# Performance work log

Hardware: AMD Instinct MI355X
Metric: run time of the kernel (lower is better)

## Reference

```python
import jax, jax.numpy as jnp
import numpy as np

N = 100000
R = 32
E = 3200000
EMB = 128
H = 32
B = 16
C = 16

def setup_inputs() -> dict:
    key = jax.random.key(0)
    ks = jax.random.split(key, 10)
    def xavier(k, shape):
        fan_in, fan_out = shape[-2], shape[-1]
        gain = jnp.sqrt(2.0)  # relu gain
        std = gain * jnp.sqrt(2.0 / (fan_in + fan_out))
        return jax.random.normal(k, shape, jnp.float32) * std
    return {
        'embeddings': xavier(ks[0], (N, EMB)),
        'comps1': xavier(ks[1], (R, B)),
        'bases1': xavier(ks[2], (B, EMB, H)),
        'comps2': xavier(ks[3], (R, B)),
        'bases2': xavier(ks[4], (B, H, C)),
        'bias1': jnp.zeros((H,), jnp.float32),
        'bias2': jnp.zeros((C,), jnp.float32),
        'rel': jax.random.randint(ks[5], (E,), 0, R, jnp.int32),
        'fr': jax.random.randint(ks[6], (E,), 0, N, jnp.int32),
        'to': jax.random.randint(ks[7], (E,), 0, N, jnp.int32),
    }

def reference(embeddings, comps1, bases1, comps2, bases2, bias1, bias2, rel, fr, to):
    n, emb = embeddings.shape
    r = comps1.shape[0]
    h = bases1.shape[2]
    # edge normalization: vals = 1 / rowsum of vertical adjacency, row = rel*n + fr
    seg = rel * n + fr  # [E]
    deg = jax.ops.segment_sum(jnp.ones_like(fr, jnp.float32), seg, num_segments=r * n)
    vals = 1.0 / deg[seg]  # [E]
    # layer 1: basis-composed weights, per-relation transform, hor-graph spmm
    w1 = jnp.einsum('rb,beh->reh', comps1, bases1)          # [r,emb,h]
    xw = jnp.einsum('ne,reh->rnh', embeddings, w1)           # [r,n,h]
    # hor_graph @ xw.view(r*n,h): hidden1[fr] += vals * xw[rel, to]
    hidden1 = jax.ops.segment_sum(vals[:, None] * xw[rel, to], fr, num_segments=n)  # [n,h]
    hidden1 = jax.nn.relu(hidden1 + bias1)
    # layer 2: ver-graph spmm then relation-combining einsum
    w2 = jnp.einsum('rb,bhc->rhc', comps2, bases2)           # [r,h,c]
    hidden2 = jax.ops.segment_sum(vals[:, None] * hidden1[to], seg, num_segments=r * n)
    hidden2 = hidden2.reshape(r, n, h)
    out = jnp.einsum('rhc,rnh->nc', w2, hidden2)             # [n,c]
    return out + bias2
```

## Files before the change

### kernel.cpp

```cpp
#include <hip/hip_runtime.h>

#define N_NODES 100000
#define N_PAD   100096
#define E_EDGES 3200000
#define NB      392
#define BCAP    12288
#define EPB     2048

typedef float f32x4 __attribute__((ext_vector_type(4)));
typedef __bf16 bf16x8 __attribute__((ext_vector_type(8)));

__device__ __forceinline__ float b2f(unsigned int u) {
    union { unsigned int i; float f; } x; x.i = u << 16; return x.f;
}
__device__ __forceinline__ unsigned short f2b(float f) {
    union { float f; unsigned int i; } x; x.f = f;
    unsigned int u = x.i + 0x7FFFu + ((x.i >> 16) & 1u);
    return (unsigned short)(u >> 16);
}

__global__ __launch_bounds__(256) void kcur(int* __restrict__ gCursor) {
    int id = blockIdx.x * 256 + threadIdx.x;
    if (id < NB) gCursor[id] = id * BCAP;
}

__global__ __launch_bounds__(256) void kemb(const float* __restrict__ emb,
                                            unsigned short* __restrict__ embb) {
    int id = blockIdx.x * 256 + threadIdx.x;
    if (id >= N_PAD * 128 / 8) return;
    size_t base = (size_t)id * 8;
    ushort4 o0 = {0, 0, 0, 0}, o1 = {0, 0, 0, 0};
    if (base < (size_t)N_NODES * 128) {
        float4 v0 = *(const float4*)(emb + base);
        float4 v1 = *(const float4*)(emb + base + 4);
        o0.x = f2b(v0.x); o0.y = f2b(v0.y); o0.z = f2b(v0.z); o0.w = f2b(v0.w);
        o1.x = f2b(v1.x); o1.y = f2b(v1.y); o1.z = f2b(v1.z); o1.w = f2b(v1.w);
    }
    *(ushort4*)(embb + base) = o0;
    *(ushort4*)(embb + base + 4) = o1;
}

__global__ __launch_bounds__(256) void kw1(const float* __restrict__ comps1,
                                           const float* __restrict__ bases1,
                                           unsigned short* __restrict__ w1T) {
    int id = blockIdx.x * 256 + threadIdx.x;
    if (id >= 1024 * 128) return;
    int k = id & 127, j = id >> 7;
    int r = j >> 5, h = j & 31;
    float s = 0.f;
#pragma unroll
    for (int b = 0; b < 16; b++)
        s += comps1[r * 16 + b] * bases1[b * 4096 + k * 32 + h];
    w1T[(size_t)j * 128 + k] = f2b(s);
}

__global__ __launch_bounds__(256) void kw2(const float* __restrict__ comps2,
                                           const float* __restrict__ bases2,
                                           unsigned short* __restrict__ w2T) {
    int id = blockIdx.x * 256 + threadIdx.x;
    if (id >= 512 * 32) return;
    int h = id & 31, j = id >> 5;
    int r = j >> 4, c = j & 15;
    float s = 0.f;
#pragma unroll
    for (int b = 0; b < 16; b++)
        s += comps2[r * 16 + b] * bases2[b * 512 + h * 16 + c];
    w2T[(size_t)j * 32 + h] = f2b(s);
}

__global__ __launch_bounds__(256) void kbinA(const int* __restrict__ rel,
                                             const int* __restrict__ fr,
                                             const int* __restrict__ to,
                                             int* __restrict__ gCursor,
                                             unsigned int* __restrict__ stage) {
    __shared__ int cnt[NB];
    __shared__ int base[NB];
    int tid = threadIdx.x;
    int g0 = blockIdx.x * (EPB / 4);
    for (int i = tid; i < NB; i += 256) cnt[i] = 0;
    __syncthreads();
#pragma unroll
    for (int i = 0; i < EPB / 1024; i++) {
        int g = g0 + i * 256 + tid;
        if (g < E_EDGES / 4) {
            int4 f4 = ((const int4*)fr)[g];
            atomicAdd(&cnt[f4.x >> 8], 1);
            atomicAdd(&cnt[f4.y >> 8], 1);
            atomicAdd(&cnt[f4.z >> 8], 1);
            atomicAdd(&cnt[f4.w >> 8], 1);
        }
    }
    __syncthreads();
    for (int i = tid; i < NB; i += 256) {
        base[i] = atomicAdd(&gCursor[i], cnt[i]);
        cnt[i] = 0;
    }
    __syncthreads();
#pragma unroll
    for (int i = 0; i < EPB / 1024; i++) {
        int g = g0 + i * 256 + tid;
        if (g < E_EDGES / 4) {
            int4 f4 = ((const int4*)fr)[g];
            int4 r4 = ((const int4*)rel)[g];
            int4 t4 = ((const int4*)to)[g];
            int fa[4] = {f4.x, f4.y, f4.z, f4.w};
            int ra[4] = {r4.x, r4.y, r4.z, r4.w};
            int ta[4] = {t4.x, t4.y, t4.z, t4.w};
#pragma unroll
            for (int u = 0; u < 4; u++) {
                int b = fa[u] >> 8;
                int rank = atomicAdd(&cnt[b], 1);
                stage[base[b] + rank] =
                    ((unsigned int)(fa[u] & 255) << 22) | ((unsigned int)ra[u] << 17) | (unsigned int)ta[u];
            }
        }
    }
}

__global__ __launch_bounds__(512) void kscan(const int* __restrict__ gCursor,
                                             int* __restrict__ bucketBase) {
    __shared__ int a[512], b[512];
    int t = threadIdx.x;
    int v = (t < NB) ? (gCursor[t] - t * BCAP) : 0;
    a[t] = v;
    __syncthreads();
    int* src = a; int* dst = b;
    for (int ofs = 1; ofs < 512; ofs <<= 1) {
        int x = src[t];
        if (t >= ofs) x += src[t - ofs];
        __syncthreads();
        dst[t] = x;
        __syncthreads();
        int* tmp = src; src = dst; dst = tmp;
    }
    if (t < NB) bucketBase[t] = src[t] - v;
}

__global__ __launch_bounds__(256) void kscatter2(const unsigned int* __restrict__ stage,
                                                 const int* __restrict__ gCursor,
                                                 const int* __restrict__ bucketBase,
                                                 int* __restrict__ rowptr,
                                                 unsigned int* __restrict__ packed) {
    __shared__ int hist[256], hexcl[256], rk[256], sa[256], sb[256];
    __shared__ int hist2[256 * 32];
    int b = blockIdx.x, t = threadIdx.x;
    int nb = gCursor[b] - b * BCAP;
    int sbase = b * BCAP;
    int gbase = bucketBase[b];
    int nb4 = nb >> 2;
    hist[t] = 0; rk[t] = 0;
    for (int i = t; i < 256 * 32; i += 256) hist2[i] = 0;
    __syncthreads();
    for (int i4 = t; i4 < nb4; i4 += 256) {
        uint4 p4 = ((const uint4*)(stage + sbase))[i4];
        unsigned int pa[4] = {p4.x, p4.y, p4.z, p4.w};
#pragma unroll
        for (int u = 0; u < 4; u++) {
            atomicAdd(&hist[pa[u] >> 22], 1);
            atomicAdd(&hist2[((pa[u] >> 22) << 5) | ((pa[u] >> 17) & 31)], 1);
        }
    }
    for (int i = (nb4 << 2) + t; i < nb; i += 256) {
        unsigned int pk = stage[sbase + i];
        atomicAdd(&hist[pk >> 22], 1);
        atomicAdd(&hist2[((pk >> 22) << 5) | ((pk >> 17) & 31)], 1);
    }
    __syncthreads();
    int v = hist[t];
    sa[t] = v;
    __syncthreads();
    int* src = sa; int* dst = sb;
    for (int ofs = 1; ofs < 256; ofs <<= 1) {
        int x = src[t];
        if (t >= ofs) x += src[t - ofs];
        __syncthreads();
        dst[t] = x;
        __syncthreads();
        int* tmp = src; src = dst; dst = tmp;
    }
    int excl = src[t] - v;
    hexcl[t] = excl;
    rowptr[b * 256 + t] = gbase + excl;
    __syncthreads();
    for (int i4 = t; i4 < nb4; i4 += 256) {
        uint4 p4 = ((const uint4*)(stage + sbase))[i4];
        unsigned int pa[4] = {p4.x, p4.y, p4.z, p4.w};
#pragma unroll
        for (int u = 0; u < 4; u++) {
            int frlo = pa[u] >> 22;
            int rank = atomicAdd(&rk[frlo], 1);
            int dg = min(hist2[(frlo << 5) | ((pa[u] >> 17) & 31)], 1023);
            packed[gbase + hexcl[frlo] + rank] = ((unsigned int)dg << 22) | (pa[u] & 0x3FFFFFu);
        }
    }
    for (int i = (nb4 << 2) + t; i < nb; i += 256) {
        unsigned int pk = stage[sbase + i];
        int frlo = pk >> 22;
        int rank = atomicAdd(&rk[frlo], 1);
        int dg = min(hist2[(frlo << 5) | ((pk >> 17) & 31)], 1023);
        packed[gbase + hexcl[frlo] + rank] = ((unsigned int)dg << 22) | (pk & 0x3FFFFFu);
    }
}

__global__ __launch_bounds__(256) void gemm1(const unsigned short* __restrict__ embb,
                                             const unsigned short* __restrict__ w1T,
                                             unsigned short* __restrict__ xw) {
    __shared__ unsigned short ldsT[4 * 16 * 136];
    int id = blockIdx.x;
    int xcd = id & 7, w = id >> 3;
    int bn = w & 15, mgl = w >> 4;
    int mg = mgl * 8 + xcd;
    if (mg >= 98) return;
    int lane = threadIdx.x & 63, wave = threadIdx.x >> 6;
    int m_ = lane & 15, q = lane >> 4;
    unsigned short* tw = &ldsT[wave * 16 * 136];
    bf16x8 B[4][4];
    const unsigned short* Bbase = w1T + (size_t)(bn * 64 + m_) * 128 + q * 8;
#pragma unroll
    for (int j = 0; j < 4; j++)
#pragma unroll
        for (int k0 = 0; k0 < 4; k0++)
            B[j][k0] = *(const bf16x8*)(Bbase + j * 16 * 128 + k0 * 32);
    int mrow0 = mg * 1024 + wave * 16;
    const unsigned short* Abase = embb + (size_t)(mrow0 + m_) * 128 + q * 8;
    bf16x8 a0[4], a1[4];
    if (mrow0 < N_PAD) {
#pragma unroll
        for (int k0 = 0; k0 < 4; k0++)
            a0[k0] = *(const bf16x8*)(Abase + k0 * 32);
    }
#pragma unroll
    for (int t = 0; t < 16; t++) {
        int m0 = mrow0 + t * 64;
        if (m0 >= N_PAD) break;
        bf16x8* acur = (t & 1) ? a1 : a0;
        bf16x8* anext = (t & 1) ? a0 : a1;
        if (t < 15 && m0 + 64 < N_PAD) {
#pragma unroll
            for (int k0 = 0; k0 < 4; k0++)
                anext[k0] = *(const bf16x8*)(Abase + (size_t)(t + 1) * 64 * 128 + k0 * 32);
        }
        f32x4 acc[4] = {};
#pragma unroll
        for (int k0 = 0; k0 < 4; k0++)
#pragma unroll
            for (int j = 0; j < 4; j++)
                acc[j] = __builtin_amdgcn_mfma_f32_16x16x32_bf16(B[j][k0], acur[k0], acc[j], 0, 0, 0);
#pragma unroll
        for (int jj = 0; jj < 4; jj++) {
            ushort4 s;
            s.x = f2b(acc[jj][0]); s.y = f2b(acc[jj][1]);
            s.z = f2b(acc[jj][2]); s.w = f2b(acc[jj][3]);
            *(ushort4*)(tw + m_ * 136 + jj * 16 + q * 4) = s;
        }
        __asm__ volatile("s_waitcnt lgkmcnt(0)" ::: "memory");
#pragma unroll
        for (int ri = 0; ri < 2; ri++) {
            int row = (lane >> 3) + ri * 8;
            int c = lane & 7;
            uint4 v = *(const uint4*)(tw + row * 136 + c * 8);
            int grow = m0 + row;
            if (grow < N_NODES)
                *(uint4*)(xw + (size_t)grow * 1024 + bn * 64 + c * 8) = v;
        }
        __asm__ volatile("s_waitcnt lgkmcnt(0)" ::: "memory");
    }
}

__global__ __launch_bounds__(256) void edge1csr(const unsigned int* __restrict__ packed,
                                                const int* __restrict__ rowptr,
                                                const unsigned short* __restrict__ xw,
                                                const float* __restrict__ bias1,
                                                unsigned short* __restrict__ h1b) {
    __shared__ unsigned int ebuf[4 * 64];
    __shared__ float vbuf[4 * 64];
    int wave = threadIdx.x >> 6, lane = threadIdx.x & 63;
    int f = blockIdx.x * 4 + wave;
    if (f >= N_NODES) return;
    int s = rowptr[f], k = rowptr[f + 1] - s;
    int sub = lane & 7, p = lane >> 3;
    f32x4 acc = {0.f, 0.f, 0.f, 0.f};
    for (int base = 0; base < k; base += 64) {
        int e = base + lane;
        if (e < k) {
            unsigned int pk = packed[s + e];
            ebuf[wave * 64 + lane] = pk;
            vbuf[wave * 64 + lane] = 1.0f / (float)(pk >> 22);
        }
        int cnum = min(64, k - base);
        int nst = (cnum + 7) >> 3;
#pragma unroll 4
        for (int i = 0; i < nst; i++) {
            int ei = (i << 3) + p;
            if (ei < cnum) {
                unsigned int pk = ebuf[wave * 64 + ei];
                float v = vbuf[wave * 64 + ei];
                int t_ = pk & 0x1FFFF, r = (pk >> 17) & 31;
                ushort4 raw = *(const ushort4*)(xw + (size_t)t_ * 1024 + (r << 5) + (sub << 2));
                acc.x += v * b2f(raw.x); acc.y += v * b2f(raw.y);
                acc.z += v * b2f(raw.z); acc.w += v * b2f(raw.w);
            }
        }
    }
#pragma unroll
    for (int ofs = 8; ofs < 64; ofs <<= 1) {
        acc.x += __shfl_xor(acc.x, ofs, 64);
        acc.y += __shfl_xor(acc.y, ofs, 64);
        acc.z += __shfl_xor(acc.z, ofs, 64);
        acc.w += __shfl_xor(acc.w, ofs, 64);
    }
    if (p == 0) {
        int h = sub << 2;
        ushort4 o;
        o.x = f2b(fmaxf(acc.x + bias1[h + 0], 0.f));
        o.y = f2b(fmaxf(acc.y + bias1[h + 1], 0.f));
        o.z = f2b(fmaxf(acc.z + bias1[h + 2], 0.f));
        o.w = f2b(fmaxf(acc.w + bias1[h + 3], 0.f));
        *(ushort4*)(h1b + (size_t)f * 32 + h) = o;
    }
}

__global__ __launch_bounds__(256) void gemm2(const unsigned short* __restrict__ h1b,
                                             const unsigned short* __restrict__ w2T,
                                             unsigned short* __restrict__ z) {
    __shared__ unsigned short ldsT[4 * 16 * 136];
    int id = blockIdx.x;
    int xcd = id & 7, w = id >> 3;
    int bn = w & 7, mgl = w >> 3;
    int mg = mgl * 8 + xcd;
    if (mg >= 98) return;
    int lane = threadIdx.x & 63, wave = threadIdx.x >> 6;
    int m_ = lane & 15, q = lane >> 4;
    unsigned short* tw = &ldsT[wave * 16 * 136];
    bf16x8 B[4];
    const unsigned short* Bbase = w2T + (size_t)(bn * 64 + m_) * 32 + q * 8;
#pragma unroll
    for (int j = 0; j < 4; j++)
        B[j] = *(const bf16x8*)(Bbase + j * 16 * 32);
    int mrow0 = mg * 1024 + wave * 32;
    const unsigned short* Abase = h1b + (size_t)(mrow0 + m_) * 32 + q * 8;
    bf16x8 a0[2], a1[2];
    if (mrow0 < N_PAD) {
        a0[0] = *(const bf16x8*)(Abase);
        a0[1] = *(const bf16x8*)(Abase + 16 * 32);
    }
#pragma unroll
    for (int t = 0; t < 8; t++) {
        int m0 = mrow0 + t * 128;
        if (m0 >= N_PAD) break;
        bf16x8* acur = (t & 1) ? a1 : a0;
        bf16x8* anext = (t & 1) ? a0 : a1;
        if (t < 7 && m0 + 128 < N_PAD) {
            anext[0] = *(const bf16x8*)(Abase + (size_t)(t + 1) * 128 * 32);
            anext[1] = *(const bf16x8*)(Abase + (size_t)(t + 1) * 128 * 32 + 16 * 32);
        }
        f32x4 acc[2][4] = {};
#pragma unroll
        for (int i = 0; i < 2; i++)
#pragma unroll
            for (int j = 0; j < 4; j++)
                acc[i][j] = __builtin_amdgcn_mfma_f32_16x16x32_bf16(B[j], acur[i], acc[i][j], 0, 0, 0);
#pragma unroll
        for (int i = 0; i < 2; i++) {
#pragma unroll
            for (int jj = 0; jj < 4; jj++) {
                ushort4 s;
                s.x = f2b(acc[i][jj][0]); s.y = f2b(acc[i][jj][1]);
                s.z = f2b(acc[i][jj][2]); s.w = f2b(acc[i][jj][3]);
                *(ushort4*)(tw + m_ * 136 + jj * 16 + q * 4) = s;
            }
            __asm__ volatile("s_waitcnt lgkmcnt(0)" ::: "memory");
#pragma unroll
            for (int ri = 0; ri < 2; ri++) {
                int row = (lane >> 3) + ri * 8;
                int c = lane & 7;
                uint4 v = *(const uint4*)(tw + row * 136 + c * 8);
                int grow = m0 + i * 16 + row;
                if (grow < N_NODES)
                    *(uint4*)(z + (size_t)grow * 512 + bn * 64 + c * 8) = v;
            }
            __asm__ volatile("s_waitcnt lgkmcnt(0)" ::: "memory");
        }
    }
}

__global__ __launch_bounds__(256) void edge2csr(const unsigned int* __restrict__ packed,
                                                const int* __restrict__ rowptr,
                                                const unsigned short* __restrict__ z,
                                                const float* __restrict__ bias2,
                                                float* __restrict__ out) {
    __shared__ unsigned int ebuf[4 * 64];
    __shared__ float vbuf[4 * 64];
    int wave = threadIdx.x >> 6, lane = threadIdx.x & 63;
    int f = blockIdx.x * 4 + wave;
    if (f >= N_NODES) return;
    int s = rowptr[f], k = rowptr[f + 1] - s;
    int sub = lane & 3, p = lane >> 2;
    f32x4 acc = {0.f, 0.f, 0.f, 0.f};
    for (int base = 0; base < k; base += 64) {
        int e = base + lane;
        if (e < k) {
            unsigned int pk = packed[s + e];
            ebuf[wave * 64 + lane] = pk;
            vbuf[wave * 64 + lane] = 1.0f / (float)(pk >> 22);
        }
        int cnum = min(64, k - base);
        int nst = (cnum + 15) >> 4;
#pragma unroll 4
        for (int i = 0; i < nst; i++) {
            int ei = (i << 4) + p;
            if (ei < cnum) {
                unsigned int pk = ebuf[wave * 64 + ei];
                float v = vbuf[wave * 64 + ei];
                int t_ = pk & 0x1FFFF, r = (pk >> 17) & 31;
                ushort4 raw = *(const ushort4*)(z + (size_t)t_ * 512 + (r << 4) + (sub << 2));
                acc.x += v * b2f(raw.x); acc.y += v * b2f(raw.y);
                acc.z += v * b2f(raw.z); acc.w += v * b2f(raw.w);
            }
        }
    }
#pragma unroll
    for (int ofs = 4; ofs < 64; ofs <<= 1) {
        acc.x += __shfl_xor(acc.x, ofs, 64);
        acc.y += __shfl_xor(acc.y, ofs, 64);
        acc.z += __shfl_xor(acc.z, ofs, 64);
        acc.w += __shfl_xor(acc.w, ofs, 64);
    }
    if (p == 0) {
        int c = sub << 2;
        float4 o;
        o.x = acc.x + bias2[c + 0];
        o.y = acc.y + bias2[c + 1];
        o.z = acc.z + bias2[c + 2];
        o.w = acc.w + bias2[c + 3];
        *(float4*)(out + (size_t)f * 16 + c) = o;
    }
}

extern "C" void kernel_launch(void* const* d_in, const int* in_sizes, int n_in,
                              void* d_out, int out_size, void* d_ws, size_t ws_size,
                              hipStream_t stream) {
    (void)in_sizes; (void)n_in; (void)out_size; (void)ws_size;
    const float* emb    = (const float*)d_in[0];
    const float* comps1 = (const float*)d_in[1];
    const float* bases1 = (const float*)d_in[2];
    const float* comps2 = (const float*)d_in[3];
    const float* bases2 = (const float*)d_in[4];
    const float* bias1  = (const float*)d_in[5];
    const float* bias2  = (const float*)d_in[6];
    const int* rel = (const int*)d_in[7];
    const int* fr  = (const int*)d_in[8];
    const int* to  = (const int*)d_in[9];
    float* out = (float*)d_out;
    char* ws = (char*)d_ws;

    int* gCursor         = (int*)(ws);
    int* bucketBase      = (int*)(ws + 2048);
    int* rowptr          = (int*)(ws + 4096);
    unsigned int* packed = (unsigned int*)(ws + 406528);
    unsigned short* h1b  = (unsigned short*)(ws + 13206528);
    unsigned short* w1T  = (unsigned short*)(ws + 19612672);
    unsigned short* w2T  = (unsigned short*)(ws + 19874816);
    unsigned short* embb = (unsigned short*)(ws + 19907584);
    unsigned short* xw   = (unsigned short*)(ws + 45532160);
    unsigned short* z    = xw;
    unsigned int* stage  = (unsigned int*)xw;

    kcur<<<2, 256, 0, stream>>>(gCursor);
    kemb<<<6256, 256, 0, stream>>>(emb, embb);
    kw1<<<512, 256, 0, stream>>>(comps1, bases1, w1T);
    kw2<<<64, 256, 0, stream>>>(comps2, bases2, w2T);
    kbinA<<<(E_EDGES + EPB - 1) / EPB, 256, 0, stream>>>(rel, fr, to, gCursor, stage);
    kscan<<<1, 512, 0, stream>>>(gCursor, bucketBase);
    kscatter2<<<NB, 256, 0, stream>>>(stage, gCursor, bucketBase, rowptr, packed);
    gemm1<<<1664, 256, 0, stream>>>(embb, w1T, xw);
    edge1csr<<<25000, 256, 0, stream>>>(packed, rowptr, xw, bias1, h1b);
    gemm2<<<832, 256, 0, stream>>>(h1b, w2T, z);
    edge2csr<<<25000, 256, 0, stream>>>(packed, rowptr, z, bias2, out);
}
```

Measured before the change: 468.1 us.

## Sort edges in LDS per block before writing buckets for coalesced stores

The binning kernel now processes 8192 edges per block, reading each edge's fields only once and holding them in registers. Each block counts edges per bucket, scans the counts, reserves global space per bucket, and scatters edges into a shared-memory sort buffer. One wavefront per bucket then copies each contiguous run to the global stage array. This replaces per-edge scattered global writes with mostly contiguous ones. In exchange it uses more registers and shared memory (32 KB sort buffer), which lowers occupancy, and adds an in-block scan with extra barriers.

```diff
diff --git a/kernel.cpp b/kernel.cpp
--- a/kernel.cpp
+++ b/kernel.cpp
@@ -5,7 +5,7 @@
 #define E_EDGES 3200000
 #define NB      392
 #define BCAP    12288
-#define EPB     2048
+#define EPB     8192
 
 typedef float f32x4 __attribute__((ext_vector_type(4)));
 typedef __bf16 bf16x8 __attribute__((ext_vector_type(8)));
@@ -74,46 +74,78 @@
                                              int* __restrict__ gCursor,
                                              unsigned int* __restrict__ stage) {
     __shared__ int cnt[NB];
-    __shared__ int base[NB];
+    __shared__ int lexcl[NB + 1];
+    __shared__ int sdelta[NB];
+    __shared__ int sa[512], sb_[512];
+    __shared__ unsigned int sortbuf[EPB];
     int tid = threadIdx.x;
-    int g0 = blockIdx.x * (EPB / 4);
+    int g40 = blockIdx.x * (EPB / 4);
+    unsigned int w_[32];
+    int bk[32];
     for (int i = tid; i < NB; i += 256) cnt[i] = 0;
     __syncthreads();
 #pragma unroll
-    for (int i = 0; i < EPB / 1024; i++) {
-        int g = g0 + i * 256 + tid;
-        if (g < E_EDGES / 4) {
-            int4 f4 = ((const int4*)fr)[g];
-            atomicAdd(&cnt[f4.x >> 8], 1);
-            atomicAdd(&cnt[f4.y >> 8], 1);
-            atomicAdd(&cnt[f4.z >> 8], 1);
-            atomicAdd(&cnt[f4.w >> 8], 1);
-        }
-    }
-    __syncthreads();
-    for (int i = tid; i < NB; i += 256) {
-        base[i] = atomicAdd(&gCursor[i], cnt[i]);
-        cnt[i] = 0;
-    }
-    __syncthreads();
-#pragma unroll
-    for (int i = 0; i < EPB / 1024; i++) {
-        int g = g0 + i * 256 + tid;
-        if (g < E_EDGES / 4) {
-            int4 f4 = ((const int4*)fr)[g];
-            int4 r4 = ((const int4*)rel)[g];
-            int4 t4 = ((const int4*)to)[g];
+    for (int i = 0; i < 8; i++) {
+        int g4 = g40 + i * 256 + tid;
+        if (g4 < E_EDGES / 4) {
+            int4 f4 = ((const int4*)fr)[g4];
+            int4 r4 = ((const int4*)rel)[g4];
+            int4 t4 = ((const int4*)to)[g4];
             int fa[4] = {f4.x, f4.y, f4.z, f4.w};
             int ra[4] = {r4.x, r4.y, r4.z, r4.w};
             int ta[4] = {t4.x, t4.y, t4.z, t4.w};
 #pragma unroll
             for (int u = 0; u < 4; u++) {
                 int b = fa[u] >> 8;
-                int rank = atomicAdd(&cnt[b], 1);
-                stage[base[b] + rank] =
-                    ((unsigned int)(fa[u] & 255) << 22) | ((unsigned int)ra[u] << 17) | (unsigned int)ta[u];
+                w_[i * 4 + u] = ((unsigned int)(fa[u] & 255) << 22) |
+                                ((unsigned int)ra[u] << 17) | (unsigned int)ta[u];
+                bk[i * 4 + u] = b;
+                atomicAdd(&cnt[b], 1);
             }
-        }
+        } else {
+#pragma unroll
+            for (int u = 0; u < 4; u++) bk[i * 4 + u] = -1;
+        }
+    }
+    __syncthreads();
+    sa[tid] = (tid < NB) ? cnt[tid] : 0;
+    sa[tid + 256] = (tid + 256 < NB) ? cnt[tid + 256] : 0;
+    __syncthreads();
+    int* src = sa; int* dst = sb_;
+    for (int ofs = 1; ofs < 512; ofs <<= 1) {
+        int x0 = src[tid];
+        if (tid >= ofs) x0 += src[tid - ofs];
+        int x1 = src[tid + 256] + src[tid + 256 - ofs];
+        __syncthreads();
+        dst[tid] = x0; dst[tid + 256] = x1;
+        __syncthreads();
+        int* tmp = src; src = dst; dst = tmp;
+    }
+    for (int b = tid; b < NB; b += 256) {
+        int c = cnt[b];
+        int lex = src[b] - c;
+        lexcl[b] = lex;
+        int gb = 0;
+        if (c) gb = atomicAdd(&gCursor[b], c);
+        sdelta[b] = gb - lex;
+        cnt[b] = 0;
+    }
+    if (tid == 0) lexcl[NB] = src[NB - 1];
+    __syncthreads();
+#pragma unroll
+    for (int i = 0; i < 32; i++) {
+        if (bk[i] >= 0) {
+            int rank = atomicAdd(&cnt[bk[i]], 1);
+            sortbuf[lexcl[bk[i]] + rank] = w_[i];
+        }
+    }
+    __syncthreads();
+    int wv = tid >> 6, lane = tid & 63;
+    for (int b = wv; b < NB; b += 4) {
+        int s = lexcl[b], e = lexcl[b + 1];
+        int d = sdelta[b];
+        for (int i = s + lane; i < e; i += 64)
+            stage[d + i] = sortbuf[i];
     }
 }
 
```

New measurement: 425.5 us. 9.1% less time.
